# Kernel tuning notes

Measured on AMD Instinct MI355X. Metric: run time of the kernel, lower is better.

Reference implementation:

```python
import jax, jax.numpy as jnp
import numpy as np

BETA = 0.9
THRESHOLD = 1.0


def setup_inputs() -> dict:
    key = jax.random.key(0)
    k1, k2 = jax.random.split(key)
    T, N_IN, N_OUT = 1024, 4096, 4096
    x = jax.random.normal(k1, (T, N_IN), dtype=jnp.float32)
    # fc1 weight initialized uniform[0,1), shape [out, in] like nn.Linear
    W = jax.random.uniform(k2, (N_OUT, N_IN), dtype=jnp.float32)
    return {"x": x, "W": W}


def reference(x, W):
    # Precompute the batched linear projection over all timesteps: [T, N_OUT]
    cur = jnp.einsum('ti,oi->to', x, W)
    mem0 = jnp.zeros((W.shape[0],), dtype=x.dtype)

    def step(mem, c):
        # snntorch Leaky, reset_mechanism='subtract':
        # reset is computed from the PREVIOUS membrane potential (detached)
        reset = (mem > THRESHOLD).astype(mem.dtype)
        mem_new = BETA * mem + c - reset * THRESHOLD
        spk = (mem_new > THRESHOLD).astype(mem.dtype)
        return mem_new, (spk, mem_new)

    _, (spk_rec, mem_rec) = jax.lax.scan(step, mem0, cur)
    return spk_rec, mem_rec
```

## Files before the change

### kernel.cpp

```cpp
#include <hip/hip_runtime.h>
#include <hip/hip_bf16.h>
#include <stdint.h>


typedef __attribute__((ext_vector_type(8))) short bf16x8;
typedef __attribute__((ext_vector_type(4))) float floatx4;

#define T_STEPS 1024
#define N_IN    4096
#define N_OUT   4096

#define GM 64
#define GN 128
#define BKK 64

#define CHUNK 32
#define NCHUNK (T_STEPS / CHUNK)

__device__ __forceinline__ unsigned short f2bf_rne(float f) {
    unsigned int u = __builtin_bit_cast(unsigned int, f);
    unsigned int r = 0x7FFFu + ((u >> 16) & 1u);
    return (unsigned short)((u + r) >> 16);
}

__global__ __launch_bounds__(256) void cvt_kernel(const float4* __restrict__ in,
                                                  ushort4* __restrict__ out, int n4) {
    int i = blockIdx.x * blockDim.x + threadIdx.x;
    if (i < n4) {
        float4 v = in[i];
        ushort4 o;
        o.x = f2bf_rne(v.x);
        o.y = f2bf_rne(v.y);
        o.z = f2bf_rne(v.z);
        o.w = f2bf_rne(v.w);
        out[i] = o;
    }
}

__device__ __forceinline__ void gload16(const void* g, void* l) {
    __builtin_amdgcn_global_load_lds((const __attribute__((address_space(1))) void*)g,
                                     (__attribute__((address_space(3))) void*)l,
                                     16, 0, 0);
}

__global__ __launch_bounds__(256) void gemm_bt(const short* __restrict__ A,
                                               const short* __restrict__ B,
                                               float* __restrict__ Ct) {
    __shared__ short sA[GM * BKK];
    __shared__ short sB[GN * BKK];
    __shared__ float sT[32 * 68];

    const int tid  = threadIdx.x;
    const int lane = tid & 63;
    const int wv   = tid >> 6;
    const int wn   = wv * 32;

    const int n_tile = blockIdx.x & 31;
    const int m_tile = blockIdx.x >> 5;
    const long bm = (long)m_tile * GM;
    const long bn = (long)n_tile * GN;

    floatx4 acc[4][2] = {};

    const int srow = tid >> 3;
    const int scol = (tid & 7) * 8;
    const short* gA[2];
    const short* gB[4];
    short* lA[2];
    short* lB[4];
#pragma unroll
    for (int p = 0; p < 2; ++p) {
        gA[p] = A + (bm + p * 32 + srow) * (long)N_IN + scol;
        lA[p] = sA + p * 2048 + tid * 8;
    }
#pragma unroll
    for (int p = 0; p < 4; ++p) {
        gB[p] = B + (bn + p * 32 + srow) * (long)N_IN + scol;
        lB[p] = sB + p * 2048 + tid * 8;
    }

    const int fm  = lane & 15;
    const int fko = (lane >> 4) * 8;

    for (int k0 = 0; k0 < N_IN; k0 += BKK) {
#pragma unroll
        for (int p = 0; p < 2; ++p) gload16(gA[p] + k0, lA[p]);
#pragma unroll
        for (int p = 0; p < 4; ++p) gload16(gB[p] + k0, lB[p]);
        __syncthreads();

#pragma unroll
        for (int ks = 0; ks < 2; ++ks) {
            bf16x8 af[4], bfr[2];
#pragma unroll
            for (int i = 0; i < 4; ++i)
                af[i] = *(const bf16x8*)(sA + (i * 16 + fm) * 64 + ks * 32 + fko);
#pragma unroll
            for (int j = 0; j < 2; ++j)
                bfr[j] = *(const bf16x8*)(sB + (wn + j * 16 + fm) * 64 + ks * 32 + fko);
#pragma unroll
            for (int i = 0; i < 4; ++i)
#pragma unroll
                for (int j = 0; j < 2; ++j)
                    acc[i][j] = __builtin_amdgcn_mfma_f32_16x16x32_bf16(
                        af[i], bfr[j], acc[i][j], 0, 0, 0);
        }
        __syncthreads();
    }

    const int cn = lane & 15;
    const int cm = (lane >> 4) * 4;
    const int trow = tid >> 3;
    const int tcol = (tid & 7) * 8;

#pragma unroll
    for (int p = 0; p < 4; ++p) {
        if (wv == p) {
#pragma unroll
            for (int j = 0; j < 2; ++j)
#pragma unroll
                for (int i = 0; i < 4; ++i)
#pragma unroll
                    for (int r = 0; r < 4; ++r)
                        sT[(j * 16 + cn) * 68 + i * 16 + cm + r] = acc[i][j][r];
        }
        __syncthreads();
#pragma unroll
        for (int q = 0; q < 2; ++q) {
            float4 v = *(const float4*)&sT[trow * 68 + tcol + q * 4];
            *(float4*)&Ct[(bn + p * 32 + trow) * (long)T_STEPS + bm + tcol + q * 4] = v;
        }
        __syncthreads();
    }
}

__global__ __launch_bounds__(64, 1) void boundary_kernel(const float* __restrict__ Ct,
                                                         float* __restrict__ bnd) {
    const int n = blockIdx.x * 64 + threadIdx.x;
    const float4* __restrict__ p4 = (const float4*)(Ct + (size_t)n * T_STEPS);

    float mem = 0.0f;
    float4 b[2][16];

#pragma unroll
    for (int j = 0; j < 16; ++j) b[0][j] = p4[j];

#pragma unroll
    for (int g = 0; g < 16; ++g) {
        const int cb = g & 1;
        if (g + 1 < 16) {
#pragma unroll
            for (int j = 0; j < 16; ++j) b[cb ^ 1][j] = p4[(g + 1) * 16 + j];
        }
        bnd[(size_t)(2 * g) * N_OUT + n] = mem;
#pragma unroll
        for (int j = 0; j < 16; ++j) {
            if (j == 8) bnd[(size_t)(2 * g + 1) * N_OUT + n] = mem;
            float cv[4] = {b[cb][j].x, b[cb][j].y, b[cb][j].z, b[cb][j].w};
#pragma unroll
            for (int e = 0; e < 4; ++e) {
                float rst = mem > 1.0f ? 1.0f : 0.0f;
                mem = 0.9f * mem + cv[e] - rst;
            }
        }
    }
}

__global__ __launch_bounds__(256) void replay_kernel(const float* __restrict__ Ct,
                                                     const float* __restrict__ bnd,
                                                     float* __restrict__ out) {
    const int lane = threadIdx.x & 63;
    const int w    = threadIdx.x >> 6;
    const int n    = blockIdx.x * 64 + lane;
    const int c    = blockIdx.y * 4 + w;
    float* __restrict__ spk  = out;
    float* __restrict__ memo = out + (size_t)T_STEPS * N_OUT;

    float mem = bnd[(size_t)c * N_OUT + n];
    const float4* __restrict__ p4 = (const float4*)(Ct + (size_t)n * T_STEPS + c * CHUNK);

    float4 v[8];
#pragma unroll
    for (int j = 0; j < 8; ++j) v[j] = p4[j];

#pragma unroll
    for (int j = 0; j < 8; ++j) {
        float cv[4] = {v[j].x, v[j].y, v[j].z, v[j].w};
#pragma unroll
        for (int e = 0; e < 4; ++e) {
            float rst = mem > 1.0f ? 1.0f : 0.0f;
            mem = 0.9f * mem + cv[e] - rst;
            size_t idx = (size_t)(c * CHUNK + j * 4 + e) * N_OUT + n;
            spk[idx]  = mem > 1.0f ? 1.0f : 0.0f;
            memo[idx] = mem;
        }
    }
}

extern "C" void kernel_launch(void* const* d_in, const int* in_sizes, int n_in,
                              void* d_out, int out_size, void* d_ws, size_t ws_size,
                              hipStream_t stream) {
    const float* x = (const float*)d_in[0];
    const float* W = (const float*)d_in[1];
    float* out = (float*)d_out;

    char* ws = (char*)d_ws;
    const size_t xbBytes  = (size_t)T_STEPS * N_IN * 2;
    const size_t WbBytes  = (size_t)N_OUT * N_IN * 2;
    const size_t CtBytes  = (size_t)N_OUT * T_STEPS * 4;
    short* xb  = (short*)ws;
    short* Wb  = (short*)(ws + xbBytes);
    float* cur = (float*)(ws + xbBytes + WbBytes);
    float* bnd = (float*)(ws + xbBytes + WbBytes + CtBytes);

    {
        int n4 = T_STEPS * N_IN / 4;
        cvt_kernel<<<n4 / 256, 256, 0, stream>>>((const float4*)x, (ushort4*)xb, n4);
    }
    {
        int n4 = N_OUT * N_IN / 4;
        cvt_kernel<<<n4 / 256, 256, 0, stream>>>((const float4*)W, (ushort4*)Wb, n4);
    }

    gemm_bt<<<(N_OUT / GN) * (T_STEPS / GM), 256, 0, stream>>>(xb, Wb, cur);

    boundary_kernel<<<N_OUT / 64, 64, 0, stream>>>(cur, bnd);

    replay_kernel<<<dim3(N_OUT / 64, NCHUNK / 4), 256, 0, stream>>>(cur, bnd, out);
}
```

Measured before the change: 203.0 us.

## Store GEMM output time-major and restructure boundary scan with LDS producer/consumer

The GEMM now writes its result directly in [T, N_OUT] row-major order instead of transposing through shared memory. The boundary scan is rewritten so three producer waves stage 128-timestep tiles for 16 neurons into a double-buffered LDS ring while one wave runs the sequential recurrence. This spreads the scan over 256 blocks instead of 64. The replay kernel now reads the time-major layout with coalesced per-timestep loads. The intent is to remove the GEMM epilogue transpose and to hide global-load latency in the serial scan, at the cost of only 16 lanes doing scan work per block and uncoalesced-width GEMM stores.

```diff
diff --git a/kernel.cpp b/kernel.cpp
--- a/kernel.cpp
+++ b/kernel.cpp
@@ -16,6 +16,10 @@
 
 #define CHUNK 32
 #define NCHUNK (T_STEPS / CHUNK)
+
+#define PH_T 128
+#define NB_N 16
+#define TP   130
 
 __device__ __forceinline__ unsigned short f2bf_rne(float f) {
     unsigned int u = __builtin_bit_cast(unsigned int, f);
@@ -45,10 +49,9 @@
 
 __global__ __launch_bounds__(256) void gemm_bt(const short* __restrict__ A,
                                                const short* __restrict__ B,
-                                               float* __restrict__ Ct) {
+                                               float* __restrict__ C) {
     __shared__ short sA[GM * BKK];
     __shared__ short sB[GN * BKK];
-    __shared__ float sT[32 * 68];
 
     const int tid  = threadIdx.x;
     const int lane = tid & 63;
@@ -110,63 +113,93 @@
 
     const int cn = lane & 15;
     const int cm = (lane >> 4) * 4;
-    const int trow = tid >> 3;
-    const int tcol = (tid & 7) * 8;
-
-#pragma unroll
-    for (int p = 0; p < 4; ++p) {
-        if (wv == p) {
-#pragma unroll
-            for (int j = 0; j < 2; ++j)
-#pragma unroll
-                for (int i = 0; i < 4; ++i)
-#pragma unroll
-                    for (int r = 0; r < 4; ++r)
-                        sT[(j * 16 + cn) * 68 + i * 16 + cm + r] = acc[i][j][r];
+#pragma unroll
+    for (int i = 0; i < 4; ++i)
+#pragma unroll
+        for (int j = 0; j < 2; ++j)
+#pragma unroll
+            for (int r = 0; r < 4; ++r)
+                C[(bm + i * 16 + cm + r) * (long)N_OUT + bn + wn + j * 16 + cn] =
+                    acc[i][j][r];
+}
+
+__global__ __launch_bounds__(256) void boundary_kernel(const float* __restrict__ cur,
+                                                       float* __restrict__ bnd) {
+    __shared__ float ring[2][NB_N * TP];
+
+    const int tid  = threadIdx.x;
+    const int wv   = tid >> 6;
+    const int lane = tid & 63;
+    const int n0   = blockIdx.x * NB_N;
+
+    const int pn = lane & 15;
+    const int tr = lane >> 4;
+
+    float mem = 0.0f;
+
+    if (wv < 3) {
+        float v[11];
+        int gidx[11];
+#pragma unroll
+        for (int i = 0; i < 11; ++i) {
+            int g = wv + 3 * i;
+            gidx[i] = g;
+            if (g < 32)
+                v[i] = cur[(size_t)(g * 4 + tr) * N_OUT + n0 + pn];
+        }
+#pragma unroll
+        for (int i = 0; i < 11; ++i)
+            if (gidx[i] < 32)
+                ring[0][pn * TP + gidx[i] * 4 + tr] = v[i];
+    }
+    __syncthreads();
+
+    for (int ph = 0; ph < T_STEPS / PH_T; ++ph) {
+        if (wv < 3) {
+            if (ph + 1 < T_STEPS / PH_T) {
+                const size_t tb = (size_t)(ph + 1) * PH_T;
+                float v[11];
+                int gidx[11];
+#pragma unroll
+                for (int i = 0; i < 11; ++i) {
+                    int g = wv + 3 * i;
+                    gidx[i] = g;
+                    if (g < 32)
+                        v[i] = cur[(tb + g * 4 + tr) * N_OUT + n0 + pn];
+                }
+#pragma unroll
+                for (int i = 0; i < 11; ++i)
+                    if (gidx[i] < 32)
+                        ring[(ph + 1) & 1][pn * TP + gidx[i] * 4 + tr] = v[i];
+            }
+        } else {
+            const float* base = &ring[ph & 1][pn * TP];
+#pragma unroll
+            for (int sub = 0; sub < 4; ++sub) {
+                if (lane < 16)
+                    bnd[(size_t)(ph * 4 + sub) * N_OUT + n0 + pn] = mem;
+                float2 buf[16];
+#pragma unroll
+                for (int q = 0; q < 16; ++q)
+                    buf[q] = *(const float2*)&base[sub * 32 + q * 2];
+#pragma unroll
+                for (int q = 0; q < 16; ++q) {
+                    {
+                        float rst = mem > 1.0f ? 1.0f : 0.0f;
+                        mem = fmaf(0.9f, mem, buf[q].x) - rst;
+                    }
+                    {
+                        float rst = mem > 1.0f ? 1.0f : 0.0f;
+                        mem = fmaf(0.9f, mem, buf[q].y) - rst;
+                    }
+                }
+            }
         }
         __syncthreads();
-#pragma unroll
-        for (int q = 0; q < 2; ++q) {
-            float4 v = *(const float4*)&sT[trow * 68 + tcol + q * 4];
-            *(float4*)&Ct[(bn + p * 32 + trow) * (long)T_STEPS + bm + tcol + q * 4] = v;
-        }
-        __syncthreads();
-    }
-}
-
-__global__ __launch_bounds__(64, 1) void boundary_kernel(const float* __restrict__ Ct,
-                                                         float* __restrict__ bnd) {
-    const int n = blockIdx.x * 64 + threadIdx.x;
-    const float4* __restrict__ p4 = (const float4*)(Ct + (size_t)n * T_STEPS);
-
-    float mem = 0.0f;
-    float4 b[2][16];
-
-#pragma unroll
-    for (int j = 0; j < 16; ++j) b[0][j] = p4[j];
-
-#pragma unroll
-    for (int g = 0; g < 16; ++g) {
-        const int cb = g & 1;
-        if (g + 1 < 16) {
-#pragma unroll
-            for (int j = 0; j < 16; ++j) b[cb ^ 1][j] = p4[(g + 1) * 16 + j];
-        }
-        bnd[(size_t)(2 * g) * N_OUT + n] = mem;
-#pragma unroll
-        for (int j = 0; j < 16; ++j) {
-            if (j == 8) bnd[(size_t)(2 * g + 1) * N_OUT + n] = mem;
-            float cv[4] = {b[cb][j].x, b[cb][j].y, b[cb][j].z, b[cb][j].w};
-#pragma unroll
-            for (int e = 0; e < 4; ++e) {
-                float rst = mem > 1.0f ? 1.0f : 0.0f;
-                mem = 0.9f * mem + cv[e] - rst;
-            }
-        }
-    }
-}
-
-__global__ __launch_bounds__(256) void replay_kernel(const float* __restrict__ Ct,
+    }
+}
+
+__global__ __launch_bounds__(256) void replay_kernel(const float* __restrict__ cur,
                                                      const float* __restrict__ bnd,
                                                      float* __restrict__ out) {
     const int lane = threadIdx.x & 63;
@@ -177,23 +210,19 @@
     float* __restrict__ memo = out + (size_t)T_STEPS * N_OUT;
 
     float mem = bnd[(size_t)c * N_OUT + n];
-    const float4* __restrict__ p4 = (const float4*)(Ct + (size_t)n * T_STEPS + c * CHUNK);
-
-    float4 v[8];
-#pragma unroll
-    for (int j = 0; j < 8; ++j) v[j] = p4[j];
-
-#pragma unroll
-    for (int j = 0; j < 8; ++j) {
-        float cv[4] = {v[j].x, v[j].y, v[j].z, v[j].w};
-#pragma unroll
-        for (int e = 0; e < 4; ++e) {
-            float rst = mem > 1.0f ? 1.0f : 0.0f;
-            mem = 0.9f * mem + cv[e] - rst;
-            size_t idx = (size_t)(c * CHUNK + j * 4 + e) * N_OUT + n;
-            spk[idx]  = mem > 1.0f ? 1.0f : 0.0f;
-            memo[idx] = mem;
-        }
+    const float* __restrict__ p = cur + (size_t)c * CHUNK * N_OUT + n;
+
+    float v[CHUNK];
+#pragma unroll
+    for (int j = 0; j < CHUNK; ++j) v[j] = p[(size_t)j * N_OUT];
+
+#pragma unroll
+    for (int j = 0; j < CHUNK; ++j) {
+        float rst = mem > 1.0f ? 1.0f : 0.0f;
+        mem = fmaf(0.9f, mem, v[j]) - rst;
+        size_t idx = (size_t)(c * CHUNK + j) * N_OUT + n;
+        spk[idx]  = mem > 1.0f ? 1.0f : 0.0f;
+        memo[idx] = mem;
     }
 }
 
@@ -205,9 +234,9 @@
     float* out = (float*)d_out;
 
     char* ws = (char*)d_ws;
-    const size_t xbBytes  = (size_t)T_STEPS * N_IN * 2;
-    const size_t WbBytes  = (size_t)N_OUT * N_IN * 2;
-    const size_t CtBytes  = (size_t)N_OUT * T_STEPS * 4;
+    const size_t xbBytes = (size_t)T_STEPS * N_IN * 2;
+    const size_t WbBytes = (size_t)N_OUT * N_IN * 2;
+    const size_t CtBytes = (size_t)T_STEPS * N_OUT * 4;
     short* xb  = (short*)ws;
     short* Wb  = (short*)(ws + xbBytes);
     float* cur = (float*)(ws + xbBytes + WbBytes);
@@ -224,7 +253,7 @@
 
     gemm_bt<<<(N_OUT / GN) * (T_STEPS / GM), 256, 0, stream>>>(xb, Wb, cur);
 
-    boundary_kernel<<<N_OUT / 64, 64, 0, stream>>>(cur, bnd);
+    boundary_kernel<<<N_OUT / NB_N, 256, 0, stream>>>(cur, bnd);
 
     replay_kernel<<<dim3(N_OUT / 64, NCHUNK / 4), 256, 0, stream>>>(cur, bnd, out);
 }
```

After: 203.5 us. No clear change (+0.3%).
